# Optimization experiments

Hardware: AMD Instinct MI355X
Metric: run time of the kernel (lower is better)

## Reference

```python
import jax, jax.numpy as jnp
import numpy as np

DT_MIN, DT_MAX = 0.001, 0.1
CHUNK = 64


def setup_inputs() -> dict:
    key = jax.random.key(0)
    ks = jax.random.split(key, 8)
    b, L, D = 2, 4096, 1024
    d_inner, d_state, nheads, K = 2048, 128, 32, 4
    conv_dim = d_inner + 2 * d_state            # 2304
    d_in_proj = 2 * d_inner + 2 * d_state + nheads  # 4384
    f32 = jnp.float32
    return {
        'x': jax.random.normal(ks[0], (b, L, D), f32),
        'in_proj_w': jax.random.normal(ks[1], (d_in_proj, D), f32) * (D ** -0.5),
        'conv_w': jax.random.normal(ks[2], (conv_dim, K), f32) * 0.3,
        'conv_b': jnp.zeros((conv_dim,), f32),
        'dt_bias': jax.random.normal(ks[3], (nheads,), f32) * 0.5,
        'A_log': jnp.log(jax.random.uniform(ks[4], (nheads,), f32, 1.0, 16.0)),
        'D_skip': jnp.ones((nheads,), f32),
        'norm_w': jnp.ones((d_inner,), f32),
        'out_proj_w': jax.random.normal(ks[5], (D, d_inner), f32) * (d_inner ** -0.5),
        'ln_w': jnp.ones((D,), f32),
        'ln_b': jnp.zeros((D,), f32),
    }


def reference(x, in_proj_w, conv_w, conv_b, dt_bias, A_log, D_skip, norm_w, out_proj_w, ln_w, ln_b):
    b, L, d_model = x.shape
    d_inner = norm_w.shape[0]
    nheads = A_log.shape[0]
    hd = d_inner // nheads                      # headdim = 64
    conv_dim = conv_w.shape[0]
    d_state = (conv_dim - d_inner) // 2
    Q = CHUNK
    c = L // Q

    # ---- Mamba2 in_proj ----
    zxbcdt = jnp.einsum('bld,kd->blk', x, in_proj_w)
    z = zxbcdt[..., :d_inner]                                   # gate
    xBC = zxbcdt[..., d_inner:d_inner + conv_dim]
    dt_raw = zxbcdt[..., d_inner + conv_dim:]                   # (b,L,h)

    # ---- causal depthwise conv1d (kernel 4) + SiLU ----
    K = conv_w.shape[1]
    xp = jnp.pad(xBC, ((0, 0), (K - 1, 0), (0, 0)))
    conv = sum(xp[:, k:k + L, :] * conv_w[:, k] for k in range(K)) + conv_b
    xBC = jax.nn.silu(conv)
    x_ssm = xBC[..., :d_inner]
    Bm = xBC[..., d_inner:d_inner + d_state]                    # (b,L,n)
    Cm = xBC[..., d_inner + d_state:]                           # (b,L,n)

    # ---- bounded dt (sigmoid, per SSMBlock fix) ----
    dt = DT_MIN + (DT_MAX - DT_MIN) * jax.nn.sigmoid(dt_raw + dt_bias)  # (b,L,h)
    A = -jnp.exp(A_log)                                          # (h,)

    # ---- chunked SSD selective scan ----
    xh = x_ssm.reshape(b, c, Q, nheads, hd)
    dtc = dt.reshape(b, c, Q, nheads)
    x_dt = xh * dtc[..., None]
    dA = jnp.einsum('bcqh,h->bhcq', dtc, A)
    Acum = jnp.cumsum(dA, axis=-1)                               # (b,h,c,Q)
    Bc = Bm.reshape(b, c, Q, d_state)
    Cc = Cm.reshape(b, c, Q, d_state)

    # intra-chunk (diagonal blocks)
    seg = Acum[..., :, None] - Acum[..., None, :]                # (b,h,c,Q,Q)
    mask = jnp.tril(jnp.ones((Q, Q), bool))
    Lmat = jnp.exp(jnp.where(mask, seg, -jnp.inf))
    Yd = jnp.einsum('bcqn,bcsn,bhcqs,bcshp->bcqhp', Cc, Bc, Lmat, x_dt)

    # chunk end-states
    decay_states = jnp.exp(Acum[..., -1:] - Acum)                # (b,h,c,Q)
    states = jnp.einsum('bcqn,bhcq,bcqhp->bchpn', Bc, decay_states, x_dt)
    chunk_decay = jnp.exp(Acum[..., -1])                         # (b,h,c)

    def step(carry, inp):
        st, dec = inp
        return dec[..., None, None] * carry + st, carry

    _, prevs = jax.lax.scan(
        step, jnp.zeros((b, nheads, hd, d_state), x.dtype),
        (jnp.moveaxis(states, 1, 0), jnp.moveaxis(chunk_decay, 2, 0)))
    prevs = jnp.moveaxis(prevs, 0, 1)                            # (b,c,h,p,n)

    # inter-chunk contribution
    Yo = jnp.einsum('bcqn,bchpn,bhcq->bcqhp', Cc, prevs, jnp.exp(Acum))

    Y = (Yd + Yo).reshape(b, L, nheads, hd) + D_skip[None, None, :, None] * xh.reshape(b, L, nheads, hd)
    y = Y.reshape(b, L, d_inner)

    # ---- gated RMSNorm + out_proj ----
    y = y * jax.nn.silu(z)
    y = y * jax.lax.rsqrt(jnp.mean(y * y, axis=-1, keepdims=True) + 1e-5) * norm_w
    out = jnp.einsum('bli,di->bld', y, out_proj_w)

    # ---- SSMBlock: LayerNorm + (eval-mode dropout) + residual ----
    mu = jnp.mean(out, axis=-1, keepdims=True)
    var = jnp.mean((out - mu) ** 2, axis=-1, keepdims=True)
    ln = (out - mu) * jax.lax.rsqrt(var + 1e-5) * ln_w + ln_b
    return x + ln
```

## Files before the change

kernel.cpp:

```cpp
#include <hip/hip_runtime.h>
#include <math.h>

#define BSZ     2
#define LEN     4096
#define DMODEL  1024
#define DINNER  2048
#define DSTATE  128
#define NHEADS  32
#define HDIM    64
#define CONVDIM 2304
#define QC      64
#define NCHUNK  64
#define ROWS    (BSZ*LEN)
#define SDIM    (HDIM*DSTATE)
#define PB      136
#define PT      72
#define CGRP    (CONVDIM/8)

typedef __attribute__((ext_vector_type(8))) short short8;
typedef __attribute__((ext_vector_type(4))) float f32x4;

__device__ __forceinline__ float silu_(float x){ return x / (1.0f + expf(-x)); }
__device__ __forceinline__ float sigm_(float x){ return 1.0f / (1.0f + expf(-x)); }
__device__ __forceinline__ float bf2f(unsigned short u){
    return __uint_as_float(((unsigned int)u) << 16);
}
__device__ __forceinline__ unsigned short f2bf(float f){
    unsigned int u = __float_as_uint(f);
    u = (u + 0x7fffu + ((u >> 16) & 1u)) >> 16;
    return (unsigned short)u;
}

__device__ __forceinline__ int swzcol(int row, int col) {
    return ((((col >> 3) ^ (row >> 3)) & 7) << 3) | (col & 7);
}
__device__ __forceinline__ int swzblk(int row, int blk) {
    return (((blk ^ (row >> 3)) & 7) << 3);
}

__device__ __forceinline__ void gload16(const void* g, void* l) {
    __builtin_amdgcn_global_load_lds(
        (const __attribute__((address_space(1))) unsigned int*)g,
        (__attribute__((address_space(3))) unsigned int*)l, 16, 0, 0);
}

__device__ __forceinline__ void cast4(const float* __restrict__ src,
                                      unsigned short* __restrict__ dst, int i) {
    const float4 v = *(const float4*)(src + (size_t)i * 4);
    ushort4 o;
    o.x = f2bf(v.x); o.y = f2bf(v.y); o.z = f2bf(v.z); o.w = f2bf(v.w);
    *(ushort4*)(dst + (size_t)i * 4) = o;
}

__global__ __launch_bounds__(256) void cast3(const float* __restrict__ s0, unsigned short* __restrict__ d0, int n0,
                                             const float* __restrict__ s1, unsigned short* __restrict__ d1, int n1,
                                             const float* __restrict__ s2, unsigned short* __restrict__ d2, int n2) {
    int i = blockIdx.x * 256 + threadIdx.x;
    if (i < n0) { cast4(s0, d0, i); return; }
    i -= n0;
    if (i < n1) { cast4(s1, d1, i); return; }
    i -= n1;
    if (i < n2) cast4(s2, d2, i);
}

__device__ __forceinline__ void stage_half(const unsigned short* __restrict__ G,
                                           void* ldsbase, int w, int lane,
                                           size_t rowbase, int lda, int kcol) {
#pragma unroll
    for (int u = 0; u < 2; u++) {
        const int f = w * 128 + u * 64 + lane;
        const int r = f >> 3;
        const int cl = (lane & 7) ^ (lane >> 3);
        gload16(G + rowbase + (size_t)r * lda + kcol + cl * 8,
                (char*)ldsbase + f * 16);
    }
}

#define WAITV(n) asm volatile("s_waitcnt vmcnt(" #n ")" ::: "memory")
#define LGKM0    asm volatile("s_waitcnt lgkmcnt(0)" ::: "memory")
#define BARRIER  do { asm volatile("" ::: "memory"); \
                      __builtin_amdgcn_s_barrier();  \
                      asm volatile("" ::: "memory"); } while (0)

#define READ_A(dst, buf, half)                                                \
    _Pragma("unroll")                                                         \
    for (int fr = 0; fr < 4; fr++) {                                          \
        const int r_ = (w & 1) * 64 + fr * 16 + l16;                          \
        _Pragma("unroll")                                                     \
        for (int s = 0; s < 2; s++)                                           \
            dst[fr][s] = *(const short8*)((const char*)&lds[buf][0][half][0]  \
                + r_ * 128 + (((s * 4 + quad) ^ rx7) << 4));                  \
    }
#define READ_B(dst, buf, half)                                                \
    _Pragma("unroll")                                                         \
    for (int fc = 0; fc < 2; fc++) {                                          \
        const int r_ = (w >> 1) * 32 + fc * 16 + l16;                         \
        _Pragma("unroll")                                                     \
        for (int s = 0; s < 2; s++)                                           \
            dst[fc][s] = *(const short8*)((const char*)&lds[buf][1][half][0]  \
                + r_ * 128 + (((s * 4 + quad) ^ rx7) << 4));                  \
    }
#define MFMA16(g, af, bfv)                                                    \
    __builtin_amdgcn_s_setprio(1);                                            \
    _Pragma("unroll")                                                         \
    for (int s = 0; s < 2; s++)                                               \
        _Pragma("unroll")                                                     \
        for (int fr = 0; fr < 4; fr++)                                        \
            _Pragma("unroll")                                                 \
            for (int fc = 0; fc < 2; fc++)                                    \
                acc[g][fr][fc] = __builtin_amdgcn_mfma_f32_16x16x32_bf16(     \
                    af[fr][s], bfv[fc][s], acc[g][fr][fc], 0, 0, 0);          \
    __builtin_amdgcn_s_setprio(0);

template<bool BF16OUT>
__device__ __forceinline__ void tile256(unsigned short (&lds)[2][2][2][8192],
                                        const unsigned short* __restrict__ Apan,
                                        const unsigned short* __restrict__ Bpan,
                                        void* __restrict__ Cout,
                                        int N, int m0, int n0,
                                        int Kfull, int kbase, int Ks) {
    const int tid = threadIdx.x;
    const int w = tid >> 6, lane = tid & 63;
    const int quad = lane >> 4, l16 = lane & 15;
    const int rx7 = l16 & 7;

    const size_t a0r = 0;
    const size_t a1r = (size_t)128 * Kfull;
    const size_t b0r = 0;
    const size_t b1r = (size_t)128 * Kfull;

    f32x4 acc[4][4][2];
#pragma unroll
    for (int g = 0; g < 4; g++)
#pragma unroll
        for (int i = 0; i < 4; i++)
#pragma unroll
            for (int j = 0; j < 2; j++) acc[g][i][j] = (f32x4){0.f, 0.f, 0.f, 0.f};

    const int NT = Ks >> 6;
    BARRIER;
    stage_half(Apan, &lds[0][0][0][0], w, lane, a0r, Kfull, kbase);
    stage_half(Bpan, &lds[0][1][0][0], w, lane, b0r, Kfull, kbase);
    stage_half(Apan, &lds[0][0][1][0], w, lane, a1r, Kfull, kbase);
    stage_half(Bpan, &lds[0][1][1][0], w, lane, b1r, Kfull, kbase);
    stage_half(Apan, &lds[1][0][0][0], w, lane, a0r, Kfull, kbase + 64);
    stage_half(Bpan, &lds[1][1][0][0], w, lane, b0r, Kfull, kbase + 64);
    stage_half(Apan, &lds[1][0][1][0], w, lane, a1r, Kfull, kbase + 64);
    WAITV(6); BARRIER;

    short8 af0[4][2], af1[4][2], bf0[2][2], bf1[2][2];
    for (int p = 0; p < (NT >> 1) - 1; p++) {
        const int kb1 = kbase + (2 * p + 1) * 64;
        const int ka2 = kbase + (2 * p + 2) * 64;
        const int kb2 = kbase + (2 * p + 3) * 64;
        READ_A(af0, 0, 0); READ_B(bf0, 0, 0);
        stage_half(Bpan, &lds[1][1][1][0], w, lane, b1r, Kfull, kb1);
        BARRIER; MFMA16(0, af0, bf0); LGKM0; BARRIER;
        READ_A(af1, 0, 1);
        stage_half(Apan, &lds[0][0][0][0], w, lane, a0r, Kfull, ka2);
        BARRIER; MFMA16(1, af1, bf0); LGKM0; BARRIER;
        READ_B(bf1, 0, 1);
        stage_half(Bpan, &lds[0][1][0][0], w, lane, b0r, Kfull, ka2);
        BARRIER; MFMA16(2, af0, bf1); LGKM0; BARRIER;
        stage_half(Apan, &lds[0][0][1][0], w, lane, a1r, Kfull, ka2);
        WAITV(6); BARRIER; MFMA16(3, af1, bf1); LGKM0; BARRIER;
        READ_A(af0, 1, 0); READ_B(bf0, 1, 0);
        stage_half(Bpan, &lds[0][1][1][0], w, lane, b1r, Kfull, ka2);
        BARRIER; MFMA16(0, af0, bf0); LGKM0; BARRIER;
        READ_A(af1, 1, 1);
        stage_half(Apan, &lds[1][0][0][0], w, lane, a0r, Kfull, kb2);
        BARRIER; MFMA16(1, af1, bf0); LGKM0; BARRIER;
        READ_B(bf1, 1, 1);
        stage_half(Bpan, &lds[1][1][0][0], w, lane, b0r, Kfull, kb2);
        BARRIER; MFMA16(2, af0, bf1); LGKM0; BARRIER;
        stage_half(Apan, &lds[1][0][1][0], w, lane, a1r, Kfull, kb2);
        WAITV(6); BARRIER; MFMA16(3, af1, bf1); LGKM0; BARRIER;
    }
    READ_A(af0, 0, 0); READ_B(bf0, 0, 0);
    stage_half(Bpan, &lds[1][1][1][0], w, lane, b1r, Kfull, kbase + (NT - 1) * 64);
    MFMA16(0, af0, bf0);
    READ_A(af1, 0, 1);
    MFMA16(1, af1, bf0);
    READ_B(bf1, 0, 1);
    MFMA16(2, af0, bf1);
    MFMA16(3, af1, bf1);
    WAITV(0); LGKM0; BARRIER;
    READ_A(af0, 1, 0); READ_B(bf0, 1, 0);
    MFMA16(0, af0, bf0);
    READ_A(af1, 1, 1);
    MFMA16(1, af1, bf0);
    READ_B(bf1, 1, 1);
    MFMA16(2, af0, bf1);
    MFMA16(3, af1, bf1);

#pragma unroll
    for (int g = 0; g < 4; g++) {
        const int qm = g & 1, qn = g >> 1;
        const int mb = m0 + qm * 128 + (w & 1) * 64;
        const int nb2 = n0 + qn * 128 + (w >> 1) * 32;
#pragma unroll
        for (int fr = 0; fr < 4; fr++)
#pragma unroll
            for (int fc = 0; fc < 2; fc++) {
                const int n = nb2 + fc * 16 + l16;
#pragma unroll
                for (int rr = 0; rr < 4; rr++) {
                    const int m = mb + fr * 16 + quad * 4 + rr;
                    if (BF16OUT)
                        ((unsigned short*)Cout)[(size_t)m * N + n] = f2bf(acc[g][fr][fc][rr]);
                    else
                        ((float*)Cout)[(size_t)m * N + n] = acc[g][fr][fc][rr];
                }
            }
    }
}

template<bool BF16OUT>
__global__ __launch_bounds__(512, 2) void gemm8p(const unsigned short* __restrict__ A,
                                                 const unsigned short* __restrict__ B,
                                                 void* __restrict__ C0,
                                                 void* __restrict__ C1,
                                                 int N, int Kfull, int Ks,
                                                 int gx, int nwg1) {
    __shared__ unsigned short lds[2][2][2][8192];
    const int nwg = gridDim.x;
    const int id = blockIdx.x;
    const int q8 = nwg >> 3, r8 = nwg & 7;
    const int xcd = id & 7, idx = id >> 3;
    const int wg = (xcd < r8 ? xcd * (q8 + 1) : r8 * (q8 + 1) + (xcd - r8) * q8) + idx;
    const int sid = wg / nwg1;
    const int wgl = wg % nwg1;
    const int m0 = (wgl / gx) * 256, n0 = (wgl % gx) * 256;
    tile256<BF16OUT>(lds, A + (size_t)m0 * Kfull, B + (size_t)n0 * Kfull,
                     sid ? C1 : C0, N, m0, n0, Kfull, sid * Ks, Ks);
}

__global__ __launch_bounds__(512, 2) void inproj_mfma(const unsigned short* __restrict__ x_bf,
                                                      const unsigned short* __restrict__ wi,
                                                      unsigned short* __restrict__ zbf,
                                                      unsigned short* __restrict__ xbc,
                                                      float* __restrict__ part0,
                                                      float* __restrict__ part1) {
    __shared__ unsigned short lds[2][2][2][8192];
    const int id = blockIdx.x;
    const int wg = (id & 7) * 32 + (id >> 3);
#pragma unroll
    for (int ti = 0; ti < 2; ti++) {
        const int t = wg + ti * 256;
        const int nt = t >> 5, mt = t & 31;
        const int m0 = mt * 256;
        const unsigned short* Apan = x_bf + (size_t)m0 * DMODEL;
        const unsigned short* Bpan = wi + (size_t)nt * 256 * DMODEL;
        if (nt < 8)
            tile256<true>(lds, Apan, Bpan, zbf, DINNER, m0, nt * 256,
                          DMODEL, 0, DMODEL);
        else
            tile256<true>(lds, Apan, Bpan, xbc, CONVDIM, m0, (nt - 8) * 256,
                          DMODEL, 0, DMODEL);
    }
    if ((wg & 3) == 0) {
        const int hi = wg >> 2;
        const int mt = hi >> 1, kh = hi & 1;
        const int m0 = mt * 256;
        tile256<false>(lds, x_bf + (size_t)m0 * DMODEL,
                       wi + (size_t)4096 * DMODEL,
                       kh ? (void*)part1 : (void*)part0, 256, m0, 0,
                       DMODEL, kh * 512, 512);
    }
}

__global__ __launch_bounds__(256) void xbc_fix(const float* __restrict__ p0,
                                               const float* __restrict__ p1,
                                               unsigned short* __restrict__ xbc) {
    const int i = (blockIdx.x * 256 + threadIdx.x) * 4;
    const int m = i >> 8, n = i & 255;
    const float4 a = *(const float4*)(p0 + i);
    const float4 b = *(const float4*)(p1 + i);
    ushort4 o;
    o.x = f2bf(a.x + b.x); o.y = f2bf(a.y + b.y);
    o.z = f2bf(a.z + b.z); o.w = f2bf(a.w + b.w);
    *(ushort4*)(xbc + (size_t)m * CONVDIM + 2048 + n) = o;
}

__global__ __launch_bounds__(256) void dtproj_mfma(const unsigned short* __restrict__ A,
                                                   const unsigned short* __restrict__ W,
                                                   const float* __restrict__ bias,
                                                   float* __restrict__ dtb,
                                                   int K) {
    __shared__ unsigned short As[4][2][32 * 32];
    __shared__ unsigned short Ws[4][2][32 * 32];
    __shared__ float red[4][32][32];
    const int tid = threadIdx.x;
    const int w = tid >> 6, lane = tid & 63;
    const int quad = lane >> 4, l16 = lane & 15;
    const int m0 = blockIdx.x * 32;
    const int kbeg = w * (1024 / 4);

    f32x4 acc[2][2];
#pragma unroll
    for (int i = 0; i < 2; i++)
#pragma unroll
        for (int j = 0; j < 2; j++) acc[i][j] = (f32x4){0.f, 0.f, 0.f, 0.f};

#define DTSTAGE(buf, kt)                                                      \
    _Pragma("unroll")                                                         \
    for (int u = 0; u < 2; u++) {                                             \
        const int f = u * 64 + lane;                                          \
        const int row = f >> 2, ke = (f & 3) * 8;                             \
        gload16(A + (size_t)(m0 + row) * K + (kt) + ke,                       \
                (char*)&As[w][buf][0] + f * 16);                              \
        gload16(W + (size_t)row * K + (kt) + ke,                              \
                (char*)&Ws[w][buf][0] + f * 16);                              \
    }

    DTSTAGE(0, kbeg);
    int buf = 0;
    for (int it = 0; it < 8; it++) {
        if (it < 7) { DTSTAGE(buf ^ 1, kbeg + (it + 1) * 32); WAITV(4); }
        else        { WAITV(0); }
        short8 af[2], bfr[2];
#pragma unroll
        for (int i = 0; i < 2; i++)
            af[i] = *(const short8*)((const char*)&As[w][buf][0] + (i * 16 + l16) * 64 + quad * 16);
#pragma unroll
        for (int j = 0; j < 2; j++)
            bfr[j] = *(const short8*)((const char*)&Ws[w][buf][0] + (j * 16 + l16) * 64 + quad * 16);
#pragma unroll
        for (int i = 0; i < 2; i++)
#pragma unroll
            for (int j = 0; j < 2; j++)
                acc[i][j] = __builtin_amdgcn_mfma_f32_16x16x32_bf16(
                    af[i], bfr[j], acc[i][j], 0, 0, 0);
        buf ^= 1;
    }
#pragma unroll
    for (int i = 0; i < 2; i++)
#pragma unroll
        for (int j = 0; j < 2; j++)
#pragma unroll
            for (int r = 0; r < 4; r++)
                red[w][i * 16 + quad * 4 + r][j * 16 + l16] = acc[i][j][r];
    __syncthreads();
#pragma unroll
    for (int e = 0; e < 4; e++) {
        const int o = tid + e * 256;
        const int m = o >> 5, hh = o & 31;
        const float v = red[0][m][hh] + red[1][m][hh] + red[2][m][hh] + red[3][m][hh];
        dtb[(size_t)m0 * NHEADS + o] = 0.001f + 0.099f * sigm_(v + bias[hh]);
    }
}

__global__ __launch_bounds__(256) void conv_silu_w(const unsigned short* __restrict__ xbc,
                                                   const float* __restrict__ cw,
                                                   const float* __restrict__ cb,
                                                   unsigned short* __restrict__ xssm,
                                                   unsigned short* __restrict__ Bb,
                                                   unsigned short* __restrict__ Cb) {
    const int idx = blockIdx.x * 256 + threadIdx.x;
    const int g = idx % CGRP;
    const int rowblk = idx / CGRP;
    const long row0 = (long)rowblk * 4;
    const int lbase = (int)(row0 & (LEN - 1));
    const int j0 = g * 8;

    float4 wv[8];
    float cbv[8];
#pragma unroll
    for (int e = 0; e < 8; e++) {
        wv[e] = *(const float4*)(cw + (size_t)(j0 + e) * 4);
        cbv[e] = cb[j0 + e];
    }

    short8 win[4];
    const short8 zero8 = (short8){0, 0, 0, 0, 0, 0, 0, 0};
#pragma unroll
    for (int t = 0; t < 3; t++) {
        const int lr = lbase - 3 + t;
        win[t] = (lr >= 0) ? *(const short8*)(xbc + (row0 - 3 + t) * CONVDIM + j0)
                           : zero8;
    }
#pragma unroll
    for (int i = 0; i < 4; i++) {
        win[3] = *(const short8*)(xbc + (row0 + i) * CONVDIM + j0);
        short8 o;
#pragma unroll
        for (int e = 0; e < 8; e++) {
            float acc = cbv[e];
            acc += bf2f((unsigned short)win[0][e]) * wv[e].x;
            acc += bf2f((unsigned short)win[1][e]) * wv[e].y;
            acc += bf2f((unsigned short)win[2][e]) * wv[e].z;
            acc += bf2f((unsigned short)win[3][e]) * wv[e].w;
            o[e] = (short)f2bf(silu_(acc));
        }
        const long row = row0 + i;
        if (j0 < DINNER)
            *(short8*)(xssm + row * DINNER + j0) = o;
        else if (j0 < DINNER + DSTATE)
            *(short8*)(Bb + row * DSTATE + (j0 - DINNER)) = o;
        else
            *(short8*)(Cb + row * DSTATE + (j0 - DINNER - DSTATE)) = o;
        win[0] = win[1]; win[1] = win[2]; win[2] = win[3];
    }
}

__global__ __launch_bounds__(256) void chunk_mfma(const unsigned short* __restrict__ xssm,
                                                  const unsigned short* __restrict__ Bb,
                                                  const unsigned short* __restrict__ Cb,
                                                  const float* __restrict__ dtb,
                                                  const float* __restrict__ A_log,
                                                  float* __restrict__ Acum,
                                                  const float* __restrict__ Dskip,
                                                  unsigned short* __restrict__ Y,
                                                  unsigned short* __restrict__ states) {
    const int c = blockIdx.x, h = blockIdx.y, b = blockIdx.z;
    const int tid = threadIdx.x;
    const int wave = tid >> 6, lane = tid & 63;
    const int quad = lane >> 4, l16 = lane & 15;

    __shared__ __attribute__((aligned(16))) unsigned short Bsh[8704];
    __shared__ __attribute__((aligned(16))) unsigned short Csh[9216];
    __shared__ __attribute__((aligned(16))) unsigned short xTs[4608];
    __shared__ float ac[QC], dts[QC], decs[QC];

    const size_t rowbase = (size_t)b * LEN + c * QC;
    if (tid < QC) {
        const float d = dtb[(rowbase + tid) * NHEADS + h];
        dts[tid] = d;
        float v = d * (-expf(A_log[h]));
#pragma unroll
        for (int off2 = 1; off2 < 64; off2 <<= 1) {
            const float nv = __shfl_up(v, off2, 64);
            if (tid >= off2) v += nv;
        }
        ac[tid] = v;
        Acum[(((size_t)b * NHEADS + h) * NCHUNK + c) * QC + tid] = v;
    }
#pragma unroll
    for (int u = 0; u < 4; u++) {
        const int vi = u * 256 + tid;
        const int s = vi >> 4, n0 = (vi & 15) * 8;
        *(short8*)&Bsh[s * PB + n0] = *(const short8*)(Bb + (rowbase + s) * DSTATE + n0);
        *(short8*)&Csh[s * PB + n0] = *(const short8*)(Cb + (rowbase + s) * DSTATE + n0);
    }
#pragma unroll
    for (int u = 0; u < 2; u++) {
        const int vi = u * 256 + tid;
        const int q = vi >> 3, p0 = (vi & 7) * 8;
        const short8 v = *(const short8*)(xssm + (rowbase + q) * DINNER + h * HDIM + p0);
#pragma unroll
        for (int j = 0; j < 8; j++) {
            const int p = p0 + j;
            xTs[p * PT + swzcol(p, q)] = (unsigned short)v[j];
        }
    }
    __syncthreads();
    if (tid < QC) decs[tid] = expf(ac[QC - 1] - ac[tid]) * dts[tid];

    f32x4 S[4];
#pragma unroll
    for (int j = 0; j < 4; j++) S[j] = (f32x4){0.f, 0.f, 0.f, 0.f};
    const int qa = wave * 16 + l16;
#pragma unroll
    for (int ks = 0; ks < 4; ks++) {
        const short8 a = *(const short8*)&Csh[qa * PB + ks * 32 + quad * 8];
#pragma unroll
        for (int j = 0; j < 4; j++) {
            const short8 bb = *(const short8*)&Bsh[(j * 16 + l16) * PB + ks * 32 + quad * 8];
            S[j] = __builtin_amdgcn_mfma_f32_16x16x32_bf16(a, bb, S[j], 0, 0, 0);
        }
    }
    unsigned short slv[4][4];
#pragma unroll
    for (int j = 0; j < 4; j++)
#pragma unroll
        for (int r = 0; r < 4; r++) {
            const int q = wave * 16 + quad * 4 + r, s = j * 16 + l16;
            const float v = (s <= q) ? S[j][r] * expf(ac[q] - ac[s]) * dts[s] : 0.f;
            slv[j][r] = f2bf(v);
        }
    __syncthreads();

    {
        const int sin = lane & 7;
        const int ng  = lane >> 3;
#pragma unroll
        for (int so = 0; so < 2; so++) {
            const int s = (wave * 2 + so) * 8 + sin;
            const float d = decs[s];
            const int cbk = s >> 3;
#pragma unroll
            for (int nh = 0; nh < 2; nh++) {
                const int noct = ng + 8 * nh;
                const int colphys = (((cbk ^ noct) & 7) << 3) | (s & 7);
#pragma unroll
                for (int j = 0; j < 8; j++) {
                    const int n = noct * 8 + ((j + sin) & 7);
                    Csh[n * PT + colphys] = f2bf(bf2f(Bsh[s * PB + n]) * d);
                }
            }
        }
    }
    __syncthreads();

#pragma unroll
    for (int j = 0; j < 4; j++)
#pragma unroll
        for (int r = 0; r < 4; r++) {
            const int row = wave * 16 + quad * 4 + r;
            const int col = j * 16 + l16;
            Bsh[row * PT + swzcol(row, col)] = slv[j][r];
        }
    __syncthreads();

    f32x4 yd[4];
#pragma unroll
    for (int j = 0; j < 4; j++) yd[j] = (f32x4){0.f, 0.f, 0.f, 0.f};
#pragma unroll
    for (int ks = 0; ks < 2; ks++) {
        const int blk = ks * 4 + quad;
        const short8 a = *(const short8*)&Bsh[qa * PT + swzblk(qa, blk)];
#pragma unroll
        for (int j = 0; j < 4; j++) {
            const int row = j * 16 + l16;
            const short8 xb = *(const short8*)&xTs[row * PT + swzblk(row, blk)];
            yd[j] = __builtin_amdgcn_mfma_f32_16x16x32_bf16(a, xb, yd[j], 0, 0, 0);
        }
    }
    const float Dh = Dskip[h];
#pragma unroll
    for (int j = 0; j < 4; j++)
#pragma unroll
        for (int r = 0; r < 4; r++) {
            const int q = wave * 16 + quad * 4 + r, p = j * 16 + l16;
            const float v = yd[j][r] + Dh * bf2f(xTs[p * PT + swzcol(p, q)]);
            Y[(rowbase + q) * DINNER + h * HDIM + p] = f2bf(v);
        }

    f32x4 st[8];
#pragma unroll
    for (int j = 0; j < 8; j++) st[j] = (f32x4){0.f, 0.f, 0.f, 0.f};
#pragma unroll
    for (int ks = 0; ks < 2; ks++) {
        const int blk = ks * 4 + quad;
        const short8 a = *(const short8*)&xTs[qa * PT + swzblk(qa, blk)];
#pragma unroll
        for (int j = 0; j < 8; j++) {
            const int row = j * 16 + l16;
            const short8 bb = *(const short8*)&Csh[row * PT + swzblk(row, blk)];
            st[j] = __builtin_amdgcn_mfma_f32_16x16x32_bf16(a, bb, st[j], 0, 0, 0);
        }
    }
    const size_t sbase = (((size_t)b * NHEADS + h) * NCHUNK + c) * SDIM;
#pragma unroll
    for (int j = 0; j < 8; j++)
#pragma unroll
        for (int r = 0; r < 4; r++) {
            const int p = wave * 16 + quad * 4 + r, n = j * 16 + l16;
            states[sbase + (size_t)p * DSTATE + n] = f2bf(st[j][r]);
        }
}

__global__ __launch_bounds__(256) void scan_kernel(unsigned short* __restrict__ states,
                                                   const float* __restrict__ Acum) {
    __shared__ float dec[NCHUNK];
    const int bh = blockIdx.y;
    const int pn = blockIdx.x * 256 + threadIdx.x;
    if (threadIdx.x < NCHUNK)
        dec[threadIdx.x] = expf(Acum[((size_t)bh * NCHUNK + threadIdx.x) * QC + (QC - 1)]);
    __syncthreads();
    float carry = 0.f;
    const size_t base = (size_t)bh * NCHUNK * SDIM + pn;
    for (int c = 0; c < NCHUNK; c++) {
        const size_t idx = base + (size_t)c * SDIM;
        const float s = bf2f(states[idx]);
        states[idx] = f2bf(carry);
        carry = dec[c] * carry + s;
    }
}

__global__ __launch_bounds__(256) void yo_mfma(const unsigned short* __restrict__ Cb,
                                               const unsigned short* __restrict__ prevs,
                                               const float* __restrict__ Acum,
                                               unsigned short* __restrict__ Y) {
    const int c = blockIdx.x, h = blockIdx.y, b = blockIdx.z;
    const int tid = threadIdx.x;
    const int wave = tid >> 6, lane = tid & 63;
    const int quad = lane >> 4, l16 = lane & 15;
    __shared__ __attribute__((aligned(16))) unsigned short Csh[8704];
    __shared__ __attribute__((aligned(16))) unsigned short Psh[8704];
    __shared__ float eq[QC];
    const size_t rowbase = (size_t)b * LEN + c * QC;
    const size_t pbase = (((size_t)b * NHEADS + h) * NCHUNK + c) * SDIM;
    if (tid < QC)
        eq[tid] = expf(Acum[(((size_t)b * NHEADS + h) * NCHUNK + c) * QC + tid]);
#pragma unroll
    for (int u = 0; u < 4; u++) {
        const int vi = u * 256 + tid;
        const int r = vi >> 4, n0 = (vi & 15) * 8;
        *(short8*)&Csh[r * PB + n0] = *(const short8*)(Cb + (rowbase + r) * DSTATE + n0);
        *(short8*)&Psh[r * PB + n0] = *(const short8*)(prevs + pbase + (size_t)r * DSTATE + n0);
    }
    __syncthreads();

    f32x4 acc[4];
#pragma unroll
    for (int j = 0; j < 4; j++) acc[j] = (f32x4){0.f, 0.f, 0.f, 0.f};
    const int qa = wave * 16 + l16;
#pragma unroll
    for (int ks = 0; ks < 4; ks++) {
        const short8 a = *(const short8*)&Csh[qa * PB + ks * 32 + quad * 8];
#pragma unroll
        for (int j = 0; j < 4; j++) {
            const short8 bb = *(const short8*)&Psh[(j * 16 + l16) * PB + ks * 32 + quad * 8];
            acc[j] = __builtin_amdgcn_mfma_f32_16x16x32_bf16(a, bb, acc[j], 0, 0, 0);
        }
    }
#pragma unroll
    for (int j = 0; j < 4; j++)
#pragma unroll
        for (int r = 0; r < 4; r++) {
            const int q = wave * 16 + quad * 4 + r, p = j * 16 + l16;
            const size_t off = (rowbase + q) * DINNER + h * HDIM + p;
            Y[off] = f2bf(bf2f(Y[off]) + eq[q] * acc[j][r]);
        }
}

__global__ __launch_bounds__(256) void gate_rms(const unsigned short* __restrict__ Y,
                                                const unsigned short* __restrict__ zbf,
                                                const float* __restrict__ nw,
                                                unsigned short* __restrict__ ybf) {
    const int r = blockIdx.x, tid = threadIdx.x;
    float4 yv[2];
    float ss = 0.f;
#pragma unroll
    for (int u = 0; u < 2; u++) {
        const int col = u * 1024 + tid * 4;
        const ushort4 y4 = *(const ushort4*)(Y + (size_t)r * DINNER + col);
        const ushort4 z4 = *(const ushort4*)(zbf + (size_t)r * DINNER + col);
        float4 y;
        y.x = bf2f(y4.x) * silu_(bf2f(z4.x)); y.y = bf2f(y4.y) * silu_(bf2f(z4.y));
        y.z = bf2f(y4.z) * silu_(bf2f(z4.z)); y.w = bf2f(y4.w) * silu_(bf2f(z4.w));
        yv[u] = y;
        ss += y.x * y.x + y.y * y.y + y.z * y.z + y.w * y.w;
    }
#pragma unroll
    for (int off = 32; off; off >>= 1) ss += __shfl_xor(ss, off, 64);
    __shared__ float red[4];
    if ((tid & 63) == 0) red[tid >> 6] = ss;
    __syncthreads();
    ss = red[0] + red[1] + red[2] + red[3];
    const float scale = rsqrtf(ss / (float)DINNER + 1e-5f);
#pragma unroll
    for (int u = 0; u < 2; u++) {
        const int col = u * 1024 + tid * 4;
        const float4 w4 = *(const float4*)(nw + col);
        ushort4 o;
        o.x = f2bf(yv[u].x * scale * w4.x); o.y = f2bf(yv[u].y * scale * w4.y);
        o.z = f2bf(yv[u].z * scale * w4.z); o.w = f2bf(yv[u].w * scale * w4.w);
        *(ushort4*)(ybf + (size_t)r * DINNER + col) = o;
    }
}

__global__ __launch_bounds__(256) void ln_res(const float* __restrict__ outb,
                                              const float* __restrict__ part,
                                              const float* __restrict__ x,
                                              const float* __restrict__ lw,
                                              const float* __restrict__ lb,
                                              float* __restrict__ out) {
    const int r = blockIdx.x, tid = threadIdx.x;
    const int col = tid * 4;
    float4 v = *(const float4*)(outb + (size_t)r * DMODEL + col);
    const float4 pv = *(const float4*)(part + (size_t)r * DMODEL + col);
    v.x += pv.x; v.y += pv.y; v.z += pv.z; v.w += pv.w;
    float s = v.x + v.y + v.z + v.w;
    float s2 = v.x * v.x + v.y * v.y + v.z * v.z + v.w * v.w;
#pragma unroll
    for (int off = 32; off; off >>= 1) {
        s += __shfl_xor(s, off, 64);
        s2 += __shfl_xor(s2, off, 64);
    }
    __shared__ float rs[4], rs2[4];
    if ((tid & 63) == 0) { rs[tid >> 6] = s; rs2[tid >> 6] = s2; }
    __syncthreads();
    s = rs[0] + rs[1] + rs[2] + rs[3];
    s2 = rs2[0] + rs2[1] + rs2[2] + rs2[3];
    const float mu = s / (float)DMODEL;
    const float var = s2 / (float)DMODEL - mu * mu;
    const float inv = rsqrtf(var + 1e-5f);
    const float4 xw = *(const float4*)(x + (size_t)r * DMODEL + col);
    const float4 w4 = *(const float4*)(lw + col);
    const float4 b4 = *(const float4*)(lb + col);
    float4 o;
    o.x = xw.x + (v.x - mu) * inv * w4.x + b4.x;
    o.y = xw.y + (v.y - mu) * inv * w4.y + b4.y;
    o.z = xw.z + (v.z - mu) * inv * w4.z + b4.z;
    o.w = xw.w + (v.w - mu) * inv * w4.w + b4.w;
    *(float4*)(out + (size_t)r * DMODEL + col) = o;
}

extern "C" void kernel_launch(void* const* d_in, const int* in_sizes, int n_in,
                              void* d_out, int out_size, void* d_ws, size_t ws_size,
                              hipStream_t stream) {
    const float* x          = (const float*)d_in[0];
    const float* in_proj_w  = (const float*)d_in[1];
    const float* conv_w     = (const float*)d_in[2];
    const float* conv_b     = (const float*)d_in[3];
    const float* dt_bias    = (const float*)d_in[4];
    const float* A_log      = (const float*)d_in[5];
    const float* D_skip     = (const float*)d_in[6];
    const float* norm_w     = (const float*)d_in[7];
    const float* out_proj_w = (const float*)d_in[8];
    const float* ln_w       = (const float*)d_in[9];
    const float* ln_b       = (const float*)d_in[10];
    float* out = (float*)d_out;
    float* ws = (float*)d_ws;

    size_t off = 0;
    unsigned short* zbf     = (unsigned short*)(ws + off); off += (size_t)ROWS * DINNER / 2;
    unsigned short* xssm_bf = (unsigned short*)(ws + off); off += (size_t)ROWS * DINNER / 2;
    unsigned short* uni     = (unsigned short*)(ws + off); off += (size_t)ROWS * CONVDIM / 2;
    unsigned short* Bb_bf   = (unsigned short*)(ws + off); off += (size_t)ROWS * DSTATE / 2;
    unsigned short* Cb_bf   = (unsigned short*)(ws + off); off += (size_t)ROWS * DSTATE / 2;
    float* dtb   = ws + off; off += (size_t)ROWS * NHEADS;
    float* Acum  = ws + off; off += (size_t)BSZ * NHEADS * NCHUNK * QC;
    unsigned short* x_bf  = (unsigned short*)(ws + off); off += (size_t)ROWS * DMODEL / 2;
    unsigned short* wi_bf = (unsigned short*)(ws + off); off += (size_t)4384 * DMODEL / 2;
    unsigned short* wo_bf = (unsigned short*)(ws + off); off += (size_t)DMODEL * DINNER / 2;
    unsigned short* states = (unsigned short*)(ws + off); off += (size_t)BSZ * NHEADS * NCHUNK * SDIM / 2;
    float* part = ws + off; off += (size_t)ROWS * DMODEL;
    const size_t need_bytes = off * sizeof(float);
    if (ws_size < need_bytes) return;

    unsigned short* xbc_bf = uni;
    unsigned short* Ybf    = uni;
    unsigned short* ybf    = xssm_bf;
    float* ip_p0 = part;
    float* ip_p1 = part + (size_t)ROWS * 256;

    {
        const int n0 = ROWS * DMODEL / 4, n1 = 4384 * DMODEL / 4, n2 = DMODEL * DINNER / 4;
        cast3<<<(n0 + n1 + n2 + 255) / 256, 256, 0, stream>>>(
            x, x_bf, n0, in_proj_w, wi_bf, n1, out_proj_w, wo_bf, n2);
    }

    inproj_mfma<<<256, 512, 0, stream>>>(x_bf, wi_bf, zbf, xbc_bf, ip_p0, ip_p1);
    xbc_fix<<<ROWS * 256 / 1024, 256, 0, stream>>>(ip_p0, ip_p1, xbc_bf);
    dtproj_mfma<<<ROWS / 32, 256, 0, stream>>>(
        x_bf, wi_bf + (size_t)(DINNER + CONVDIM) * DMODEL, dt_bias, dtb, DMODEL);

    conv_silu_w<<<(ROWS / 4) * CGRP / 256, 256, 0, stream>>>(
        xbc_bf, conv_w, conv_b, xssm_bf, Bb_bf, Cb_bf);
    chunk_mfma<<<dim3(NCHUNK, NHEADS, BSZ), 256, 0, stream>>>(
        xssm_bf, Bb_bf, Cb_bf, dtb, A_log, Acum, D_skip, Ybf, states);
    scan_kernel<<<dim3(SDIM / 256, BSZ * NHEADS), 256, 0, stream>>>(states, Acum);
    yo_mfma<<<dim3(NCHUNK, NHEADS, BSZ), 256, 0, stream>>>(Cb_bf, states, Acum, Ybf);
    gate_rms<<<ROWS, 256, 0, stream>>>(Ybf, zbf, norm_w, ybf);

    gemm8p<false><<<2 * (ROWS / 256) * (DMODEL / 256), 512, 0, stream>>>(
        ybf, wo_bf, out, part, DMODEL, DINNER, DINNER / 2,
        DMODEL / 256, (ROWS / 256) * (DMODEL / 256));
    ln_res<<<ROWS, 256, 0, stream>>>(out, part, x, ln_w, ln_b, out);
}
```

Baseline: 453.3 us.

## Split fused in-proj kernel into separate gemm8p launches per output segment

Replaces the single persistent inproj_mfma kernel, which processed two 256x256 tiles per workgroup plus a split-K tail, with three gemm8p launches: one for the z segment, one for the first 2048 xBC columns, and a split-K launch for the last 256 columns. It also removes the leading barrier in tile256 before the initial LDS staging. This trades the hand-balanced persistent schedule for more launches and simpler grids. Dropping the barrier risks an LDS race when a workgroup runs tile256 more than once, though gemm8p calls it once per block.

```diff
diff --git a/kernel.cpp b/kernel.cpp
--- a/kernel.cpp
+++ b/kernel.cpp
@@ -138,7 +138,6 @@
             for (int j = 0; j < 2; j++) acc[g][i][j] = (f32x4){0.f, 0.f, 0.f, 0.f};
 
     const int NT = Ks >> 6;
-    BARRIER;
     stage_half(Apan, &lds[0][0][0][0], w, lane, a0r, Kfull, kbase);
     stage_half(Bpan, &lds[0][1][0][0], w, lane, b0r, Kfull, kbase);
     stage_half(Apan, &lds[0][0][1][0], w, lane, a1r, Kfull, kbase);
@@ -235,40 +234,6 @@
                      sid ? C1 : C0, N, m0, n0, Kfull, sid * Ks, Ks);
 }
 
-__global__ __launch_bounds__(512, 2) void inproj_mfma(const unsigned short* __restrict__ x_bf,
-                                                      const unsigned short* __restrict__ wi,
-                                                      unsigned short* __restrict__ zbf,
-                                                      unsigned short* __restrict__ xbc,
-                                                      float* __restrict__ part0,
-                                                      float* __restrict__ part1) {
-    __shared__ unsigned short lds[2][2][2][8192];
-    const int id = blockIdx.x;
-    const int wg = (id & 7) * 32 + (id >> 3);
-#pragma unroll
-    for (int ti = 0; ti < 2; ti++) {
-        const int t = wg + ti * 256;
-        const int nt = t >> 5, mt = t & 31;
-        const int m0 = mt * 256;
-        const unsigned short* Apan = x_bf + (size_t)m0 * DMODEL;
-        const unsigned short* Bpan = wi + (size_t)nt * 256 * DMODEL;
-        if (nt < 8)
-            tile256<true>(lds, Apan, Bpan, zbf, DINNER, m0, nt * 256,
-                          DMODEL, 0, DMODEL);
-        else
-            tile256<true>(lds, Apan, Bpan, xbc, CONVDIM, m0, (nt - 8) * 256,
-                          DMODEL, 0, DMODEL);
-    }
-    if ((wg & 3) == 0) {
-        const int hi = wg >> 2;
-        const int mt = hi >> 1, kh = hi & 1;
-        const int m0 = mt * 256;
-        tile256<false>(lds, x_bf + (size_t)m0 * DMODEL,
-                       wi + (size_t)4096 * DMODEL,
-                       kh ? (void*)part1 : (void*)part0, 256, m0, 0,
-                       DMODEL, kh * 512, 512);
-    }
-}
-
 __global__ __launch_bounds__(256) void xbc_fix(const float* __restrict__ p0,
                                                const float* __restrict__ p1,
                                                unsigned short* __restrict__ xbc) {
@@ -743,7 +708,15 @@
             x, x_bf, n0, in_proj_w, wi_bf, n1, out_proj_w, wo_bf, n2);
     }
 
-    inproj_mfma<<<256, 512, 0, stream>>>(x_bf, wi_bf, zbf, xbc_bf, ip_p0, ip_p1);
+    gemm8p<true><<<(ROWS / 256) * (DINNER / 256), 512, 0, stream>>>(
+        x_bf, wi_bf, zbf, nullptr, DINNER, DMODEL, DMODEL,
+        DINNER / 256, (ROWS / 256) * (DINNER / 256));
+    gemm8p<true><<<(ROWS / 256) * 8, 512, 0, stream>>>(
+        x_bf, wi_bf + (size_t)DINNER * DMODEL, xbc_bf, nullptr, CONVDIM, DMODEL, DMODEL,
+        8, (ROWS / 256) * 8);
+    gemm8p<false><<<2 * (ROWS / 256), 512, 0, stream>>>(
+        x_bf, wi_bf + (size_t)4096 * DMODEL, ip_p0, ip_p1, 256, DMODEL, DMODEL / 2,
+        1, ROWS / 256);
     xbc_fix<<<ROWS * 256 / 1024, 256, 0, stream>>>(ip_p0, ip_p1, xbc_bf);
     dtproj_mfma<<<ROWS / 32, 256, 0, stream>>>(
         x_bf, wi_bf + (size_t)(DINNER + CONVDIM) * DMODEL, dt_bias, dtb, DMODEL);
```

Result: faster. 408.0 us (-10.0%).
